# Optimization experiments

Hardware: AMD Instinct MI355X
Metric: run time of the kernel (lower is better)

Reference implementation:

```python
import jax, jax.numpy as jnp
import numpy as np

M = 12288
B = 1
C_IN = 8
C_OUT = 16
K = 5


def setup_inputs() -> dict:
    key = jax.random.key(0)
    kL, kx, kt = jax.random.split(key, 3)
    # Scale L so its spectral radius is ~0.5, keeping L^k x numerically tame.
    L = jax.random.normal(kL, (M, M), dtype=jnp.float32) * (0.5 / np.sqrt(M))
    x = jax.random.normal(kx, (B, C_IN, M), dtype=jnp.float32)
    theta = jax.random.normal(kt, (C_OUT, C_IN, K), dtype=jnp.float32)
    bias = jnp.zeros((1, C_OUT, 1), dtype=jnp.float32)
    return {"L": L, "x": x, "theta": theta, "bias": bias}


def reference(L, x, theta, bias):
    Bb, C_in, Mm = x.shape
    Kk = theta.shape[-1]
    # Batch the shared recurrence L^k x into one (M,M)x(M,B*C_in) matmul per step.
    cur = x.reshape(Bb * C_in, Mm).T          # [M, B*C_in]
    powers = [cur]
    for _ in range(Kk - 1):                   # small fixed K, structural loop
        cur = L @ cur                         # [M, B*C_in]
        powers.append(cur)
    X = jnp.stack(powers, axis=0)             # [K, M, B*C_in]
    X = X.transpose(2, 1, 0).reshape(Bb, C_in, Mm, Kk)  # [B, C_in, M, K]
    y = jnp.einsum('bimk,oik->bom', X, theta)           # [B, C_out, M]
    return y + bias
```

## Files before the change

### kernel.cpp

```cpp
#include <hip/hip_runtime.h>
#include <hip/hip_bf16.h>

#define MM 12288
#define NCH 8
#define COUT 16
#define KK 5
#define ROWS 4

__global__ __launch_bounds__(64) void matpanel_kernel(
        const float* __restrict__ L,
        const float* __restrict__ vin,
        float* __restrict__ vout) {
    const int lane = threadIdx.x;
    const int row0 = blockIdx.x * ROWS;

    float acc[ROWS][NCH];
#pragma unroll
    for (int r = 0; r < ROWS; ++r)
#pragma unroll
        for (int c = 0; c < NCH; ++c) acc[r][c] = 0.f;

    for (int it = 0; it < MM / 256; ++it) {
        const int j = it * 256 + lane * 4;
        float4 v[NCH];
#pragma unroll
        for (int c = 0; c < NCH; ++c)
            v[c] = *(const float4*)(vin + (size_t)c * MM + j);
#pragma unroll
        for (int r = 0; r < ROWS; ++r) {
            const float4 a = *(const float4*)(L + (size_t)(row0 + r) * MM + j);
#pragma unroll
            for (int c = 0; c < NCH; ++c) {
                acc[r][c] += a.x * v[c].x + a.y * v[c].y
                           + a.z * v[c].z + a.w * v[c].w;
            }
        }
    }

    float val[ROWS * NCH];
#pragma unroll
    for (int r = 0; r < ROWS; ++r)
#pragma unroll
        for (int c = 0; c < NCH; ++c) val[r * NCH + c] = acc[r][c];

#pragma unroll
    for (int v = 0; v < 32; ++v) val[v] += __shfl_xor(val[v], 32, 64);

#pragma unroll
    for (int d = 16; d >= 1; d >>= 1) {
        const bool up = (lane & d) != 0;
#pragma unroll
        for (int v = 0; v < 16; ++v) {
            if (v < d) {
                const float keep = up ? val[v + d] : val[v];
                const float send = up ? val[v] : val[v + d];
                const float recv = __shfl_xor(send, d, 64);
                val[v] = keep + recv;
            }
        }
    }

    if (lane < 32) {
        const int r = lane >> 3;
        const int c = lane & 7;
        vout[(size_t)c * MM + row0 + r] = val[0];
    }
}

__global__ __launch_bounds__(256) void combine_kernel(
        const float* __restrict__ x,
        const float* __restrict__ P,
        const float* __restrict__ theta,
        const float* __restrict__ bias,
        float* __restrict__ y) {
    const int m = blockIdx.x * blockDim.x + threadIdx.x;
    if (m >= MM) return;

    float p[KK][NCH];
#pragma unroll
    for (int c = 0; c < NCH; ++c) p[0][c] = x[(size_t)c * MM + m];
#pragma unroll
    for (int k = 1; k < KK; ++k)
#pragma unroll
        for (int c = 0; c < NCH; ++c)
            p[k][c] = P[((size_t)(k - 1) * NCH + c) * MM + m];

#pragma unroll
    for (int o = 0; o < COUT; ++o) {
        float acc = bias[o];
#pragma unroll
        for (int c = 0; c < NCH; ++c)
#pragma unroll
            for (int k = 0; k < KK; ++k)
                acc += theta[(o * NCH + c) * KK + k] * p[k][c];
        y[(size_t)o * MM + m] = acc;
    }
}

extern "C" void kernel_launch(void* const* d_in, const int* in_sizes, int n_in,
                              void* d_out, int out_size, void* d_ws, size_t ws_size,
                              hipStream_t stream) {
    const float* L     = (const float*)d_in[0];
    const float* x     = (const float*)d_in[1];
    const float* theta = (const float*)d_in[2];
    const float* bias  = (const float*)d_in[3];
    float* out = (float*)d_out;
    float* P   = (float*)d_ws;

    const size_t S = (size_t)NCH * MM;
    const int grid = MM / ROWS;

    matpanel_kernel<<<grid, 64, 0, stream>>>(L, x,         P);
    matpanel_kernel<<<grid, 64, 0, stream>>>(L, P,         P + S);
    matpanel_kernel<<<grid, 64, 0, stream>>>(L, P + S,     P + 2 * S);
    matpanel_kernel<<<grid, 64, 0, stream>>>(L, P + 2 * S, P + 3 * S);

    combine_kernel<<<(MM + 255) / 256, 256, 0, stream>>>(x, P, theta, bias, out);
}
```

Baseline: 1.312 ms.

## Share input vector chunks across 8 waves via LDS in matvec panel kernel

Blocks now hold 8 waves, each computing 4 rows of L, and they cooperatively stage each 256-column chunk of the 8-channel vector in shared memory. Each wave loads one channel slice instead of all eight. This removes redundant vector loads from cache per wave and leaves the L stream as the dominant traffic. In exchange, it adds two block barriers per chunk, which can stall waves and reduce latency hiding.

```diff
diff --git a/kernel.cpp b/kernel.cpp
--- a/kernel.cpp
+++ b/kernel.cpp
@@ -6,13 +6,23 @@
 #define COUT 16
 #define KK 5
 #define ROWS 4
+#define WPB 8
+#define RB (ROWS * WPB)
+#define CHUNK 256
 
-__global__ __launch_bounds__(64) void matpanel_kernel(
+__global__ __launch_bounds__(512) void matpanel_kernel(
         const float* __restrict__ L,
         const float* __restrict__ vin,
         float* __restrict__ vout) {
-    const int lane = threadIdx.x;
-    const int row0 = blockIdx.x * ROWS;
+    const int tid  = threadIdx.x;
+    const int lane = tid & 63;
+    const int wave = tid >> 6;
+    const int row0 = blockIdx.x * RB + wave * ROWS;
+
+    const int sc = wave;
+    const int sj = lane * 4;
+
+    __shared__ float sv[NCH][CHUNK];
 
     float acc[ROWS][NCH];
 #pragma unroll
@@ -20,19 +30,26 @@
 #pragma unroll
         for (int c = 0; c < NCH; ++c) acc[r][c] = 0.f;
 
-    for (int it = 0; it < MM / 256; ++it) {
-        const int j = it * 256 + lane * 4;
-        float4 v[NCH];
+    for (int it = 0; it < MM / CHUNK; ++it) {
+        const int jbase = it * CHUNK;
+
+        const float4 t = *(const float4*)(vin + (size_t)sc * MM + jbase + sj);
+        float4 la[ROWS];
 #pragma unroll
-        for (int c = 0; c < NCH; ++c)
-            v[c] = *(const float4*)(vin + (size_t)c * MM + j);
+        for (int r = 0; r < ROWS; ++r)
+            la[r] = *(const float4*)(L + (size_t)(row0 + r) * MM + jbase + lane * 4);
+
+        __syncthreads();
+        *(float4*)(&sv[sc][sj]) = t;
+        __syncthreads();
+
 #pragma unroll
-        for (int r = 0; r < ROWS; ++r) {
-            const float4 a = *(const float4*)(L + (size_t)(row0 + r) * MM + j);
+        for (int c = 0; c < NCH; ++c) {
+            const float4 v = *(const float4*)(&sv[c][lane * 4]);
 #pragma unroll
-            for (int c = 0; c < NCH; ++c) {
-                acc[r][c] += a.x * v[c].x + a.y * v[c].y
-                           + a.z * v[c].z + a.w * v[c].w;
+            for (int r = 0; r < ROWS; ++r) {
+                acc[r][c] += la[r].x * v.x + la[r].y * v.y
+                           + la[r].z * v.z + la[r].w * v.w;
             }
         }
     }
@@ -108,12 +125,12 @@
     float* P   = (float*)d_ws;
 
     const size_t S = (size_t)NCH * MM;
-    const int grid = MM / ROWS;
+    const int grid = MM / RB;
 
-    matpanel_kernel<<<grid, 64, 0, stream>>>(L, x,         P);
-    matpanel_kernel<<<grid, 64, 0, stream>>>(L, P,         P + S);
-    matpanel_kernel<<<grid, 64, 0, stream>>>(L, P + S,     P + 2 * S);
-    matpanel_kernel<<<grid, 64, 0, stream>>>(L, P + 2 * S, P + 3 * S);
+    matpanel_kernel<<<grid, 512, 0, stream>>>(L, x,         P);
+    matpanel_kernel<<<grid, 512, 0, stream>>>(L, P,         P + S);
+    matpanel_kernel<<<grid, 512, 0, stream>>>(L, P + S,     P + 2 * S);
+    matpanel_kernel<<<grid, 512, 0, stream>>>(L, P + 2 * S, P + 3 * S);
 
     combine_kernel<<<(MM + 255) / 256, 256, 0, stream>>>(x, P, theta, bias, out);
 }
```

Result: faster. 1.200 ms (-8.5%).
